# Kernel optimization log

Measured on AMD Instinct MI355X. Metric: run time of the kernel, lower is better.

The kernel has to match this reference:

```python
import jax, jax.numpy as jnp
import numpy as np

GRID = 20            # grid_size -> n1 = 400 nodes
CTX = 64             # context_size
HID = 10 * CTX       # hidden_dim per module code
BATCH = 256
K_ITERS = 100        # Dykstra iterations approximating the exact QP solve
LEAKY_SLOPE = 0.1


def _grid_incidence(g):
    """Incidence matrix of g x g grid DAG with right/down edges (SPO benchmark)."""
    n1 = g * g
    edges = []
    for i in range(g):
        for j in range(g):
            u = i * g + j
            if j + 1 < g:
                edges.append((u, u + 1))   # right
            if i + 1 < g:
                edges.append((u, u + g))   # down
    n2 = len(edges)
    A = np.zeros((n1, n2), dtype=np.float32)
    for e, (u, v) in enumerate(edges):
        A[u, e] = 1.0    # flow leaves u
        A[v, e] = -1.0   # flow enters v
    b = np.zeros(n1, dtype=np.float32)
    b[0] = 1.0           # source
    b[-1] = -1.0         # sink
    return A, b


def setup_inputs() -> dict:
    key = jax.random.key(0)
    ks = jax.random.split(key, 5)
    A_np, b_np = _grid_incidence(GRID)
    n2 = A_np.shape[1]
    d = jax.random.normal(ks[0], (BATCH, CTX), dtype=jnp.float32)
    W1 = jax.random.normal(ks[1], (CTX, HID), dtype=jnp.float32) / np.sqrt(CTX)
    b1 = jax.random.normal(ks[2], (HID,), dtype=jnp.float32) * 0.01
    W2 = jax.random.normal(ks[3], (HID, n2), dtype=jnp.float32) / np.sqrt(HID)
    b2 = jax.random.normal(ks[4], (n2,), dtype=jnp.float32) * 0.01
    return {
        "d": d, "W1": W1, "b1": b1, "W2": W2, "b2": b2,
        "A": jnp.asarray(A_np), "b_eq": jnp.asarray(b_np),
    }


def _solve_qp(w, A, b_eq):
    """Batched min_x w'x + 0.5||x||^2 s.t. Ax=b, x>=0 == proj of -w onto the
    feasible set, via Dykstra alternating projections (affine set / orthant)."""
    M = jnp.linalg.pinv(A @ A.T)  # [n1, n1]; AA' is the grid Laplacian (rank n1-1)

    def proj_affine(x):           # x: [B, n2]
        resid = x @ A.T - b_eq    # [B, n1]
        return x - (resid @ M) @ A

    y0 = -w                       # point to project
    p0 = jnp.zeros_like(w)
    q0 = jnp.zeros_like(w)

    def step(carry, _):
        y, p, q = carry
        t = y + p
        yp = proj_affine(t)
        p = t - yp
        t2 = yp + q
        y = jnp.maximum(t2, 0.0)  # projection onto x >= 0
        q = t2 - y
        return (y, p, q), None

    (y, _, _), _ = jax.lax.scan(step, (y0, p0, q0), None, length=K_ITERS)
    return y


def reference(d, W1, b1, W2, b2, A, b_eq):
    h = d @ W1 + b1
    h = jnp.where(h > 0, h, LEAKY_SLOPE * h)   # LeakyReLU(0.1)
    w = h @ W2 + b2                            # predicted edge costs [B, n2]
    return _solve_qp(w, A, b_eq)               # training-mode output: QP solution
```

## Files before the change

### kernel.cpp

```cpp
#include <hip/hip_runtime.h>
#include <math.h>

#define G 20
#define N1 400
#define N2 760
#define CTXS 64
#define HID 640
#define NB 256
#define ITERS 100
#define PI_F 3.14159265358979323846f

__device__ __forceinline__ int eR(int i, int j) { return (i < 19) ? (39 * i + 2 * j) : (741 + j); }
__device__ __forceinline__ int eD(int i, int j) { return (j < 19) ? (39 * i + 2 * j + 1) : (39 * i + 38); }

#define LOAD_ROW20(dst, base) do {                                          \
    const float4* _rp = (const float4*)(base);                              \
    float4 _r0 = _rp[0], _r1 = _rp[1], _r2 = _rp[2], _r3 = _rp[3], _r4 = _rp[4]; \
    dst[0]=_r0.x; dst[1]=_r0.y; dst[2]=_r0.z; dst[3]=_r0.w;                 \
    dst[4]=_r1.x; dst[5]=_r1.y; dst[6]=_r1.z; dst[7]=_r1.w;                 \
    dst[8]=_r2.x; dst[9]=_r2.y; dst[10]=_r2.z; dst[11]=_r2.w;               \
    dst[12]=_r3.x; dst[13]=_r3.y; dst[14]=_r3.z; dst[15]=_r3.w;             \
    dst[16]=_r4.x; dst[17]=_r4.y; dst[18]=_r4.z; dst[19]=_r4.w; } while (0)

__global__ __launch_bounds__(256, 1) void spnet_kernel(
    const float* __restrict__ dmat, const float* __restrict__ W1,
    const float* __restrict__ b1v, const float* __restrict__ W2,
    const float* __restrict__ b2v, float* __restrict__ out)
{
  const int tid = threadIdx.x;
  const int bb  = blockIdx.x;

  __shared__ __align__(16) float sdrow[CTXS];
  __shared__ __align__(16) float sh[HID];
  __shared__ __align__(16) float st0[N2];
  __shared__ __align__(16) float srowT[N1];
  __shared__ __align__(16) float sc1[N1];
  __shared__ __align__(16) float sc2T[N1];
  __shared__ __align__(16) float sd1[N1];
  __shared__ __align__(16) float szz[N1];
  __shared__ __align__(16) float tRs[G][G];
  __shared__ __align__(16) float tDs[21][G];

  for (int t = tid; t < N1; t += 256) ((float*)tRs)[t] = 0.f;
  for (int t = tid; t < 21 * G; t += 256) ((float*)tDs)[t] = 0.f;
  if (tid < CTXS) sdrow[tid] = dmat[bb * CTXS + tid];

  const bool isC = (tid < 200);
  const int c  = tid / 10;
  const int u  = tid % 10;
  const int k0 = 2 * u;

  float VA0[10], VA1[10], VC[20], S0, S1;
  {
    const float n0 = 0.22360679774997896f, nk = 0.31622776601683794f;
#pragma unroll
    for (int i = 0; i < 10; ++i) {
      VA0[i] = ((k0 == 0) ? n0 : nk) * cosf((float)(k0 * (2 * i + 1)) * (PI_F / 40.f));
      VA1[i] = nk * cosf((float)((k0 + 1) * (2 * i + 1)) * (PI_F / 40.f));
    }
#pragma unroll
    for (int k = 0; k < 20; ++k)
      VC[k] = ((k == 0) ? n0 : nk) * cosf((float)(k * (2 * u + 1)) * (PI_F / 40.f));
    float lc = 2.f - 2.f * cosf((float)c * (PI_F / 20.f));
    float l0 = 2.f - 2.f * cosf((float)k0 * (PI_F / 20.f));
    float l1 = 2.f - 2.f * cosf((float)(k0 + 1) * (PI_F / 20.f));
    S0 = (c == 0 && k0 == 0) ? 0.f : 1.f / (lc + l0);
    S1 = 1.f / (lc + l1);
  }

  __syncthreads();

  if (tid < HID / 4) {
    float4 acc = *(const float4*)(b1v + 4 * tid);
#pragma unroll 4
    for (int k = 0; k < CTXS; k += 4) {
      float4 h4 = *(const float4*)(sdrow + k);
      const float* wb = W1 + k * HID + 4 * tid;
      float4 w0 = *(const float4*)(wb);
      float4 w1 = *(const float4*)(wb + HID);
      float4 w2 = *(const float4*)(wb + 2 * HID);
      float4 w3 = *(const float4*)(wb + 3 * HID);
      acc.x = fmaf(h4.x, w0.x, acc.x); acc.y = fmaf(h4.x, w0.y, acc.y);
      acc.z = fmaf(h4.x, w0.z, acc.z); acc.w = fmaf(h4.x, w0.w, acc.w);
      acc.x = fmaf(h4.y, w1.x, acc.x); acc.y = fmaf(h4.y, w1.y, acc.y);
      acc.z = fmaf(h4.y, w1.z, acc.z); acc.w = fmaf(h4.y, w1.w, acc.w);
      acc.x = fmaf(h4.z, w2.x, acc.x); acc.y = fmaf(h4.z, w2.y, acc.y);
      acc.z = fmaf(h4.z, w2.z, acc.z); acc.w = fmaf(h4.z, w2.w, acc.w);
      acc.x = fmaf(h4.w, w3.x, acc.x); acc.y = fmaf(h4.w, w3.y, acc.y);
      acc.z = fmaf(h4.w, w3.z, acc.z); acc.w = fmaf(h4.w, w3.w, acc.w);
    }
    acc.x = acc.x > 0.f ? acc.x : 0.1f * acc.x;
    acc.y = acc.y > 0.f ? acc.y : 0.1f * acc.y;
    acc.z = acc.z > 0.f ? acc.z : 0.1f * acc.z;
    acc.w = acc.w > 0.f ? acc.w : 0.1f * acc.w;
    *(float4*)(sh + 4 * tid) = acc;
  }
  __syncthreads();

  if (tid < N2 / 4) {
    float4 acc = *(const float4*)(b2v + 4 * tid);
#pragma unroll 2
    for (int k = 0; k < HID; k += 4) {
      float4 h4 = *(const float4*)(sh + k);
      const float* wb = W2 + k * N2 + 4 * tid;
      float4 w0 = *(const float4*)(wb);
      float4 w1 = *(const float4*)(wb + N2);
      float4 w2 = *(const float4*)(wb + 2 * N2);
      float4 w3 = *(const float4*)(wb + 3 * N2);
      acc.x = fmaf(h4.x, w0.x, acc.x); acc.y = fmaf(h4.x, w0.y, acc.y);
      acc.z = fmaf(h4.x, w0.z, acc.z); acc.w = fmaf(h4.x, w0.w, acc.w);
      acc.x = fmaf(h4.y, w1.x, acc.x); acc.y = fmaf(h4.y, w1.y, acc.y);
      acc.z = fmaf(h4.y, w1.z, acc.z); acc.w = fmaf(h4.y, w1.w, acc.w);
      acc.x = fmaf(h4.z, w2.x, acc.x); acc.y = fmaf(h4.z, w2.y, acc.y);
      acc.z = fmaf(h4.z, w2.z, acc.z); acc.w = fmaf(h4.z, w2.w, acc.w);
      acc.x = fmaf(h4.w, w3.x, acc.x); acc.y = fmaf(h4.w, w3.y, acc.y);
      acc.z = fmaf(h4.w, w3.z, acc.z); acc.w = fmaf(h4.w, w3.w, acc.w);
    }
    float4 s; s.x = -acc.x; s.y = -acc.y; s.z = -acc.z; s.w = -acc.w;
    *(float4*)(st0 + 4 * tid) = s;
  }

  const int  di = tid / 5, dj4 = (tid % 5) * 4;
  const bool dAct = (tid < 100) && (di < 19);
  float dT[4], dQ[4], dY[4];
  const int  rid = tid - 128;
  const bool isR = (rid >= 0 && rid < 100);
  const int  ri = isR ? (rid / 5) : 0, rj4 = isR ? ((rid % 5) * 4) : 0;
  float rT[4], rQ[4], rY[4];
#pragma unroll
  for (int m = 0; m < 4; ++m) { dT[m]=0.f; dQ[m]=0.f; dY[m]=0.f; rT[m]=0.f; rQ[m]=0.f; rY[m]=0.f; }

  __syncthreads();

  if (dAct) {
#pragma unroll
    for (int m = 0; m < 4; ++m) dT[m] = st0[eD(di, dj4 + m)];
    *(float4*)&tDs[di + 1][dj4] = make_float4(dT[0], dT[1], dT[2], dT[3]);
  }
  if (isR) {
#pragma unroll
    for (int m = 0; m < 4; ++m) {
      int j = rj4 + m;
      rT[m] = (j < 19) ? st0[eR(ri, j)] : 0.f;
    }
    *(float4*)&tRs[ri][rj4] = make_float4(rT[0], rT[1], rT[2], rT[3]);
  }
  __syncthreads();

  for (int it = 0; it < ITERS; ++it) {
    if (isR) {
      float4 oR = *(const float4*)&tRs[ri][rj4];
      float  lf = (rj4 > 0) ? tRs[ri][rj4 - 1] : 0.f;
      float4 oD = *(const float4*)&tDs[ri + 1][rj4];
      float4 iD = *(const float4*)&tDs[ri][rj4];
      float r0 = oR.x + oD.x - lf   - iD.x;
      float r1 = oR.y + oD.y - oR.x - iD.y;
      float r2 = oR.z + oD.z - oR.y - iD.z;
      float r3 = oR.w + oD.w - oR.z - iD.w;
      if (ri == 0  && rj4 == 0)  r0 -= 1.f;
      if (ri == 19 && rj4 == 16) r3 += 1.f;
      srowT[(rj4 + 0) * G + ri] = r0;
      srowT[(rj4 + 1) * G + ri] = r1;
      srowT[(rj4 + 2) * G + ri] = r2;
      srowT[(rj4 + 3) * G + ri] = r3;
    }
    __syncthreads();

    if (isC) {
      float d_[20]; LOAD_ROW20(d_, srowT + 20 * c);
      float a0 = 0.f, a1 = 0.f;
#pragma unroll
      for (int i = 0; i < 10; ++i) {
        float e_ = d_[i] + d_[19 - i], o_ = d_[i] - d_[19 - i];
        a0 = fmaf(VA0[i], e_, a0);
        a1 = fmaf(VA1[i], o_, a1);
      }
      sc1[k0 * G + c] = a0;
      sc1[(k0 + 1) * G + c] = a1;
    }
    __syncthreads();

    if (isC) {
      float d_[20]; LOAD_ROW20(d_, sc1 + 20 * c);
      float a0 = 0.f, a1 = 0.f;
#pragma unroll
      for (int j = 0; j < 10; ++j) {
        float e_ = d_[j] + d_[19 - j], o_ = d_[j] - d_[19 - j];
        a0 = fmaf(VA0[j], e_, a0);
        a1 = fmaf(VA1[j], o_, a1);
      }
      sc2T[k0 * G + c] = a0 * S0;
      sc2T[(k0 + 1) * G + c] = a1 * S1;
    }
    __syncthreads();

    if (isC) {
      float d_[20]; LOAD_ROW20(d_, sc2T + 20 * c);
      float E = 0.f, O = 0.f;
#pragma unroll
      for (int m = 0; m < 10; ++m) {
        E = fmaf(VC[2 * m], d_[2 * m], E);
        O = fmaf(VC[2 * m + 1], d_[2 * m + 1], O);
      }
      sd1[u * G + c] = E + O;
      sd1[(19 - u) * G + c] = E - O;
    }
    __syncthreads();

    if (isC) {
      float d_[20]; LOAD_ROW20(d_, sd1 + 20 * c);
      float E = 0.f, O = 0.f;
#pragma unroll
      for (int m = 0; m < 10; ++m) {
        E = fmaf(VC[2 * m], d_[2 * m], E);
        O = fmaf(VC[2 * m + 1], d_[2 * m + 1], O);
      }
      szz[c * G + u] = E + O;
      szz[c * G + (19 - u)] = E - O;
    }
    __syncthreads();

    if (isR) {
      float4 z4 = *(const float4*)&szz[ri * G + rj4];
      float  zR = (rj4 < 16) ? szz[ri * G + rj4 + 4] : 0.f;
      float pn[4] = {z4.x - z4.y, z4.y - z4.z, z4.z - z4.w, z4.w - zR};
      if (rj4 == 16) pn[3] = 0.f;
#pragma unroll
      for (int m = 0; m < 4; ++m) {
        float t2 = rT[m] - pn[m] + rQ[m];
        float yn = fmaxf(t2, 0.f);
        rQ[m] = t2 - yn; rY[m] = yn; rT[m] = yn + pn[m];
      }
      *(float4*)&tRs[ri][rj4] = make_float4(rT[0], rT[1], rT[2], rT[3]);
    }
    if (dAct) {
      float4 z4 = *(const float4*)&szz[di * G + dj4];
      float4 zb = *(const float4*)&szz[(di + 1) * G + dj4];
      float pn[4] = {z4.x - zb.x, z4.y - zb.y, z4.z - zb.z, z4.w - zb.w};
#pragma unroll
      for (int m = 0; m < 4; ++m) {
        float t2 = dT[m] - pn[m] + dQ[m];
        float yn = fmaxf(t2, 0.f);
        dQ[m] = t2 - yn; dY[m] = yn; dT[m] = yn + pn[m];
      }
      *(float4*)&tDs[di + 1][dj4] = make_float4(dT[0], dT[1], dT[2], dT[3]);
    }
    __syncthreads();
  }

  float* mine = out + bb * N2;
  if (isR) {
#pragma unroll
    for (int m = 0; m < 4; ++m) {
      int j = rj4 + m;
      if (j < 19) mine[eR(ri, j)] = rY[m];
    }
  }
  if (dAct) {
#pragma unroll
    for (int m = 0; m < 4; ++m) mine[eD(di, dj4 + m)] = dY[m];
  }
}

extern "C" void kernel_launch(void* const* d_in, const int* in_sizes, int n_in,
                              void* d_out, int out_size, void* d_ws, size_t ws_size,
                              hipStream_t stream) {
  const float* d   = (const float*)d_in[0];
  const float* W1  = (const float*)d_in[1];
  const float* b1  = (const float*)d_in[2];
  const float* W2  = (const float*)d_in[3];
  const float* b2  = (const float*)d_in[4];
  float* out = (float*)d_out;
  spnet_kernel<<<NB, 256, 0, stream>>>(d, W1, b1, W2, b2, out);
}
```

Measured before the change: 213.8 us.

## Run Dykstra iterations in a single wavefront, replacing barriers with waitcnt and shuffles

After the MLP, the block drops to one 64-lane wavefront that owns all edge state in registers and does the DCT-based Laplacian solve with each lane covering four columns. The per-stage __syncthreads barriers become s_waitcnt lgkmcnt(0), and neighbour edge values come from cross-lane shuffles instead of shared-memory tiles. This removes about six block barriers per iteration and the tRs/tDs shared buffers. In exchange, each lane does about four times more DCT work and the loop uses only one wave per CU. It also relies on LDS ordering within a single wavefront, which is implicit and fragile.

After: 324.8 us. 51.9% more time.

```diff
diff --git a/kernel.cpp b/kernel.cpp
--- a/kernel.cpp
+++ b/kernel.cpp
@@ -13,6 +13,8 @@
 __device__ __forceinline__ int eR(int i, int j) { return (i < 19) ? (39 * i + 2 * j) : (741 + j); }
 __device__ __forceinline__ int eD(int i, int j) { return (j < 19) ? (39 * i + 2 * j + 1) : (39 * i + 38); }
 
+#define WAIT_LDS() asm volatile("s_waitcnt lgkmcnt(0)" ::: "memory")
+
 #define LOAD_ROW20(dst, base) do {                                          \
     const float4* _rp = (const float4*)(base);                              \
     float4 _r0 = _rp[0], _r1 = _rp[1], _r2 = _rp[2], _r3 = _rp[3], _r4 = _rp[4]; \
@@ -22,6 +24,11 @@
     dst[12]=_r3.x; dst[13]=_r3.y; dst[14]=_r3.z; dst[15]=_r3.w;             \
     dst[16]=_r4.x; dst[17]=_r4.y; dst[18]=_r4.z; dst[19]=_r4.w; } while (0)
 
+__device__ __forceinline__ void fma4v(float4& acc, float s, const float4& v) {
+  acc.x = fmaf(s, v.x, acc.x); acc.y = fmaf(s, v.y, acc.y);
+  acc.z = fmaf(s, v.z, acc.z); acc.w = fmaf(s, v.w, acc.w);
+}
+
 __global__ __launch_bounds__(256, 1) void spnet_kernel(
     const float* __restrict__ dmat, const float* __restrict__ W1,
     const float* __restrict__ b1v, const float* __restrict__ W2,
@@ -38,36 +45,8 @@
   __shared__ __align__(16) float sc2T[N1];
   __shared__ __align__(16) float sd1[N1];
   __shared__ __align__(16) float szz[N1];
-  __shared__ __align__(16) float tRs[G][G];
-  __shared__ __align__(16) float tDs[21][G];
-
-  for (int t = tid; t < N1; t += 256) ((float*)tRs)[t] = 0.f;
-  for (int t = tid; t < 21 * G; t += 256) ((float*)tDs)[t] = 0.f;
+
   if (tid < CTXS) sdrow[tid] = dmat[bb * CTXS + tid];
-
-  const bool isC = (tid < 200);
-  const int c  = tid / 10;
-  const int u  = tid % 10;
-  const int k0 = 2 * u;
-
-  float VA0[10], VA1[10], VC[20], S0, S1;
-  {
-    const float n0 = 0.22360679774997896f, nk = 0.31622776601683794f;
-#pragma unroll
-    for (int i = 0; i < 10; ++i) {
-      VA0[i] = ((k0 == 0) ? n0 : nk) * cosf((float)(k0 * (2 * i + 1)) * (PI_F / 40.f));
-      VA1[i] = nk * cosf((float)((k0 + 1) * (2 * i + 1)) * (PI_F / 40.f));
-    }
-#pragma unroll
-    for (int k = 0; k < 20; ++k)
-      VC[k] = ((k == 0) ? n0 : nk) * cosf((float)(k * (2 * u + 1)) * (PI_F / 40.f));
-    float lc = 2.f - 2.f * cosf((float)c * (PI_F / 20.f));
-    float l0 = 2.f - 2.f * cosf((float)k0 * (PI_F / 20.f));
-    float l1 = 2.f - 2.f * cosf((float)(k0 + 1) * (PI_F / 20.f));
-    S0 = (c == 0 && k0 == 0) ? 0.f : 1.f / (lc + l0);
-    S1 = 1.f / (lc + l1);
-  }
-
   __syncthreads();
 
   if (tid < HID / 4) {
@@ -80,14 +59,8 @@
       float4 w1 = *(const float4*)(wb + HID);
       float4 w2 = *(const float4*)(wb + 2 * HID);
       float4 w3 = *(const float4*)(wb + 3 * HID);
-      acc.x = fmaf(h4.x, w0.x, acc.x); acc.y = fmaf(h4.x, w0.y, acc.y);
-      acc.z = fmaf(h4.x, w0.z, acc.z); acc.w = fmaf(h4.x, w0.w, acc.w);
-      acc.x = fmaf(h4.y, w1.x, acc.x); acc.y = fmaf(h4.y, w1.y, acc.y);
-      acc.z = fmaf(h4.y, w1.z, acc.z); acc.w = fmaf(h4.y, w1.w, acc.w);
-      acc.x = fmaf(h4.z, w2.x, acc.x); acc.y = fmaf(h4.z, w2.y, acc.y);
-      acc.z = fmaf(h4.z, w2.z, acc.z); acc.w = fmaf(h4.z, w2.w, acc.w);
-      acc.x = fmaf(h4.w, w3.x, acc.x); acc.y = fmaf(h4.w, w3.y, acc.y);
-      acc.z = fmaf(h4.w, w3.z, acc.z); acc.w = fmaf(h4.w, w3.w, acc.w);
+      fma4v(acc, h4.x, w0); fma4v(acc, h4.y, w1);
+      fma4v(acc, h4.z, w2); fma4v(acc, h4.w, w3);
     }
     acc.x = acc.x > 0.f ? acc.x : 0.1f * acc.x;
     acc.y = acc.y > 0.f ? acc.y : 0.1f * acc.y;
@@ -107,158 +80,205 @@
       float4 w1 = *(const float4*)(wb + N2);
       float4 w2 = *(const float4*)(wb + 2 * N2);
       float4 w3 = *(const float4*)(wb + 3 * N2);
-      acc.x = fmaf(h4.x, w0.x, acc.x); acc.y = fmaf(h4.x, w0.y, acc.y);
-      acc.z = fmaf(h4.x, w0.z, acc.z); acc.w = fmaf(h4.x, w0.w, acc.w);
-      acc.x = fmaf(h4.y, w1.x, acc.x); acc.y = fmaf(h4.y, w1.y, acc.y);
-      acc.z = fmaf(h4.y, w1.z, acc.z); acc.w = fmaf(h4.y, w1.w, acc.w);
-      acc.x = fmaf(h4.z, w2.x, acc.x); acc.y = fmaf(h4.z, w2.y, acc.y);
-      acc.z = fmaf(h4.z, w2.z, acc.z); acc.w = fmaf(h4.z, w2.w, acc.w);
-      acc.x = fmaf(h4.w, w3.x, acc.x); acc.y = fmaf(h4.w, w3.y, acc.y);
-      acc.z = fmaf(h4.w, w3.z, acc.z); acc.w = fmaf(h4.w, w3.w, acc.w);
+      fma4v(acc, h4.x, w0); fma4v(acc, h4.y, w1);
+      fma4v(acc, h4.z, w2); fma4v(acc, h4.w, w3);
     }
     float4 s; s.x = -acc.x; s.y = -acc.y; s.z = -acc.z; s.w = -acc.w;
     *(float4*)(st0 + 4 * tid) = s;
   }
-
-  const int  di = tid / 5, dj4 = (tid % 5) * 4;
-  const bool dAct = (tid < 100) && (di < 19);
-  float dT[4], dQ[4], dY[4];
-  const int  rid = tid - 128;
-  const bool isR = (rid >= 0 && rid < 100);
-  const int  ri = isR ? (rid / 5) : 0, rj4 = isR ? ((rid % 5) * 4) : 0;
-  float rT[4], rQ[4], rY[4];
-#pragma unroll
-  for (int m = 0; m < 4; ++m) { dT[m]=0.f; dQ[m]=0.f; dY[m]=0.f; rT[m]=0.f; rQ[m]=0.f; rY[m]=0.f; }
-
   __syncthreads();
 
-  if (dAct) {
-#pragma unroll
-    for (int m = 0; m < 4; ++m) dT[m] = st0[eD(di, dj4 + m)];
-    *(float4*)&tDs[di + 1][dj4] = make_float4(dT[0], dT[1], dT[2], dT[3]);
-  }
-  if (isR) {
-#pragma unroll
-    for (int m = 0; m < 4; ++m) {
-      int j = rj4 + m;
-      rT[m] = (j < 19) ? st0[eR(ri, j)] : 0.f;
-    }
-    *(float4*)&tRs[ri][rj4] = make_float4(rT[0], rT[1], rT[2], rT[3]);
-  }
-  __syncthreads();
+  if (tid >= 64) return;
+  const int ln = tid;
+
+  const int  r = ln >> 1, h = ln & 1, j0 = 10 * h;
+  const bool eAct = (ln < 40);
+  const bool rOK  = (r < 19);
+  float tR[10], qR[10], tD[10], qD[10], yR[10], yD[10];
+#pragma unroll
+  for (int m = 0; m < 10; ++m) { tR[m]=0.f; qR[m]=0.f; tD[m]=0.f; qD[m]=0.f; yR[m]=0.f; yD[m]=0.f; }
+  if (eAct) {
+#pragma unroll
+    for (int m = 0; m < 10; ++m) {
+      int j = j0 + m;
+      if ((h == 0) || (m < 9)) tR[m] = st0[eR(r, j)];
+      if (rOK)                 tD[m] = st0[eD(r, j)];
+    }
+  }
+
+  const bool cAct = (ln < 50);
+  int du = ln / 5; if (du > 9) du = 9;
+  const int dg = ln % 5;
+  const int k0 = 2 * du;
+  float VA0[10], VA1[10], VC[20], S0v[4], S1v[4];
+  {
+    const float n0 = 0.22360679774997896f, nk = 0.31622776601683794f;
+#pragma unroll
+    for (int i = 0; i < 10; ++i) {
+      VA0[i] = ((k0 == 0) ? n0 : nk) * cosf((float)(k0 * (2 * i + 1)) * (PI_F / 40.f));
+      VA1[i] = nk * cosf((float)((k0 + 1) * (2 * i + 1)) * (PI_F / 40.f));
+    }
+#pragma unroll
+    for (int k = 0; k < 20; ++k)
+      VC[k] = ((k == 0) ? n0 : nk) * cosf((float)(k * (2 * du + 1)) * (PI_F / 40.f));
+    float l0 = 2.f - 2.f * cosf((float)k0 * (PI_F / 20.f));
+    float l1 = 2.f - 2.f * cosf((float)(k0 + 1) * (PI_F / 20.f));
+#pragma unroll
+    for (int cc = 0; cc < 4; ++cc) {
+      int c = 4 * dg + cc;
+      float lc = 2.f - 2.f * cosf((float)c * (PI_F / 20.f));
+      S0v[cc] = (c == 0 && k0 == 0) ? 0.f : 1.f / (lc + l0);
+      S1v[cc] = 1.f / (lc + l1);
+    }
+  }
+
+  {
+    float tDup[10];
+#pragma unroll
+    for (int m = 0; m < 10; ++m) tDup[m] = __shfl(tD[m], (ln >= 2) ? ln - 2 : ln, 64);
+    float tRl = __shfl(tR[9], (ln >= 1) ? ln - 1 : ln, 64);
+    if (eAct) {
+      float rr[10];
+#pragma unroll
+      for (int m = 0; m < 10; ++m) {
+        float inR = (m == 0) ? ((h == 0) ? 0.f : tRl) : tR[m - 1];
+        float inD = (r == 0) ? 0.f : tDup[m];
+        rr[m] = tR[m] + tD[m] - inR - inD;
+      }
+      if (r == 0  && h == 0) rr[0] -= 1.f;
+      if (r == 19 && h == 1) rr[9] += 1.f;
+#pragma unroll
+      for (int m = 0; m < 10; ++m) srowT[(j0 + m) * G + r] = rr[m];
+    }
+  }
+  WAIT_LDS();
 
   for (int it = 0; it < ITERS; ++it) {
-    if (isR) {
-      float4 oR = *(const float4*)&tRs[ri][rj4];
-      float  lf = (rj4 > 0) ? tRs[ri][rj4 - 1] : 0.f;
-      float4 oD = *(const float4*)&tDs[ri + 1][rj4];
-      float4 iD = *(const float4*)&tDs[ri][rj4];
-      float r0 = oR.x + oD.x - lf   - iD.x;
-      float r1 = oR.y + oD.y - oR.x - iD.y;
-      float r2 = oR.z + oD.z - oR.y - iD.z;
-      float r3 = oR.w + oD.w - oR.z - iD.w;
-      if (ri == 0  && rj4 == 0)  r0 -= 1.f;
-      if (ri == 19 && rj4 == 16) r3 += 1.f;
-      srowT[(rj4 + 0) * G + ri] = r0;
-      srowT[(rj4 + 1) * G + ri] = r1;
-      srowT[(rj4 + 2) * G + ri] = r2;
-      srowT[(rj4 + 3) * G + ri] = r3;
-    }
-    __syncthreads();
-
-    if (isC) {
-      float d_[20]; LOAD_ROW20(d_, srowT + 20 * c);
-      float a0 = 0.f, a1 = 0.f;
-#pragma unroll
-      for (int i = 0; i < 10; ++i) {
-        float e_ = d_[i] + d_[19 - i], o_ = d_[i] - d_[19 - i];
-        a0 = fmaf(VA0[i], e_, a0);
-        a1 = fmaf(VA1[i], o_, a1);
-      }
-      sc1[k0 * G + c] = a0;
-      sc1[(k0 + 1) * G + c] = a1;
-    }
-    __syncthreads();
-
-    if (isC) {
-      float d_[20]; LOAD_ROW20(d_, sc1 + 20 * c);
-      float a0 = 0.f, a1 = 0.f;
-#pragma unroll
-      for (int j = 0; j < 10; ++j) {
-        float e_ = d_[j] + d_[19 - j], o_ = d_[j] - d_[19 - j];
-        a0 = fmaf(VA0[j], e_, a0);
-        a1 = fmaf(VA1[j], o_, a1);
-      }
-      sc2T[k0 * G + c] = a0 * S0;
-      sc2T[(k0 + 1) * G + c] = a1 * S1;
-    }
-    __syncthreads();
-
-    if (isC) {
-      float d_[20]; LOAD_ROW20(d_, sc2T + 20 * c);
-      float E = 0.f, O = 0.f;
+    if (cAct) {
+#pragma unroll
+      for (int cc = 0; cc < 4; ++cc) {
+        const int c = 4 * dg + cc;
+        float d_[20]; LOAD_ROW20(d_, srowT + 20 * c);
+        float a0 = 0.f, a1 = 0.f;
+#pragma unroll
+        for (int i = 0; i < 10; ++i) {
+          float e_ = d_[i] + d_[19 - i], o_ = d_[i] - d_[19 - i];
+          a0 = fmaf(VA0[i], e_, a0);
+          a1 = fmaf(VA1[i], o_, a1);
+        }
+        sc1[k0 * G + c] = a0;
+        sc1[(k0 + 1) * G + c] = a1;
+      }
+    }
+    WAIT_LDS();
+
+    if (cAct) {
+#pragma unroll
+      for (int cc = 0; cc < 4; ++cc) {
+        const int c = 4 * dg + cc;
+        float d_[20]; LOAD_ROW20(d_, sc1 + 20 * c);
+        float a0 = 0.f, a1 = 0.f;
+#pragma unroll
+        for (int j = 0; j < 10; ++j) {
+          float e_ = d_[j] + d_[19 - j], o_ = d_[j] - d_[19 - j];
+          a0 = fmaf(VA0[j], e_, a0);
+          a1 = fmaf(VA1[j], o_, a1);
+        }
+        sc2T[k0 * G + c] = a0 * S0v[cc];
+        sc2T[(k0 + 1) * G + c] = a1 * S1v[cc];
+      }
+    }
+    WAIT_LDS();
+
+    if (cAct) {
+#pragma unroll
+      for (int cc = 0; cc < 4; ++cc) {
+        const int c = 4 * dg + cc;
+        float d_[20]; LOAD_ROW20(d_, sc2T + 20 * c);
+        float E = 0.f, O = 0.f;
+#pragma unroll
+        for (int m = 0; m < 10; ++m) {
+          E = fmaf(VC[2 * m], d_[2 * m], E);
+          O = fmaf(VC[2 * m + 1], d_[2 * m + 1], O);
+        }
+        sd1[du * G + c] = E + O;
+        sd1[(19 - du) * G + c] = E - O;
+      }
+    }
+    WAIT_LDS();
+
+    if (cAct) {
+#pragma unroll
+      for (int cc = 0; cc < 4; ++cc) {
+        const int c = 4 * dg + cc;
+        float d_[20]; LOAD_ROW20(d_, sd1 + 20 * c);
+        float E = 0.f, O = 0.f;
+#pragma unroll
+        for (int m = 0; m < 10; ++m) {
+          E = fmaf(VC[2 * m], d_[2 * m], E);
+          O = fmaf(VC[2 * m + 1], d_[2 * m + 1], O);
+        }
+        szz[c * G + du] = E + O;
+        szz[c * G + (19 - du)] = E - O;
+      }
+    }
+    WAIT_LDS();
+
+    if (eAct) {
+      const int zb = r * G + j0;
+      float zi[11], zd[10];
+#pragma unroll
+      for (int m = 0; m < 10; ++m) zi[m] = szz[zb + m];
+      { int a10 = zb + 10; if (a10 > 399) a10 = 399; zi[10] = szz[a10]; }
+      const int zb2 = (rOK ? (r + 1) : r) * G + j0;
+#pragma unroll
+      for (int m = 0; m < 10; ++m) zd[m] = szz[zb2 + m];
 #pragma unroll
       for (int m = 0; m < 10; ++m) {
-        E = fmaf(VC[2 * m], d_[2 * m], E);
-        O = fmaf(VC[2 * m + 1], d_[2 * m + 1], O);
-      }
-      sd1[u * G + c] = E + O;
-      sd1[(19 - u) * G + c] = E - O;
-    }
-    __syncthreads();
-
-    if (isC) {
-      float d_[20]; LOAD_ROW20(d_, sd1 + 20 * c);
-      float E = 0.f, O = 0.f;
+        bool vR = (h == 0) || (m < 9);
+        float pn = vR ? (zi[m] - zi[m + 1]) : 0.f;
+        float t2 = tR[m] - pn + qR[m];
+        float yn = fmaxf(t2, 0.f);
+        qR[m] = t2 - yn; yR[m] = yn; tR[m] = yn + pn;
+      }
 #pragma unroll
       for (int m = 0; m < 10; ++m) {
-        E = fmaf(VC[2 * m], d_[2 * m], E);
-        O = fmaf(VC[2 * m + 1], d_[2 * m + 1], O);
-      }
-      szz[c * G + u] = E + O;
-      szz[c * G + (19 - u)] = E - O;
-    }
-    __syncthreads();
-
-    if (isR) {
-      float4 z4 = *(const float4*)&szz[ri * G + rj4];
-      float  zR = (rj4 < 16) ? szz[ri * G + rj4 + 4] : 0.f;
-      float pn[4] = {z4.x - z4.y, z4.y - z4.z, z4.z - z4.w, z4.w - zR};
-      if (rj4 == 16) pn[3] = 0.f;
-#pragma unroll
-      for (int m = 0; m < 4; ++m) {
-        float t2 = rT[m] - pn[m] + rQ[m];
+        float pn = rOK ? (zi[m] - zd[m]) : 0.f;
+        float t2 = tD[m] - pn + qD[m];
         float yn = fmaxf(t2, 0.f);
-        rQ[m] = t2 - yn; rY[m] = yn; rT[m] = yn + pn[m];
-      }
-      *(float4*)&tRs[ri][rj4] = make_float4(rT[0], rT[1], rT[2], rT[3]);
-    }
-    if (dAct) {
-      float4 z4 = *(const float4*)&szz[di * G + dj4];
-      float4 zb = *(const float4*)&szz[(di + 1) * G + dj4];
-      float pn[4] = {z4.x - zb.x, z4.y - zb.y, z4.z - zb.z, z4.w - zb.w};
-#pragma unroll
-      for (int m = 0; m < 4; ++m) {
-        float t2 = dT[m] - pn[m] + dQ[m];
-        float yn = fmaxf(t2, 0.f);
-        dQ[m] = t2 - yn; dY[m] = yn; dT[m] = yn + pn[m];
-      }
-      *(float4*)&tDs[di + 1][dj4] = make_float4(dT[0], dT[1], dT[2], dT[3]);
-    }
-    __syncthreads();
-  }
-
-  float* mine = out + bb * N2;
-  if (isR) {
-#pragma unroll
-    for (int m = 0; m < 4; ++m) {
-      int j = rj4 + m;
-      if (j < 19) mine[eR(ri, j)] = rY[m];
-    }
-  }
-  if (dAct) {
-#pragma unroll
-    for (int m = 0; m < 4; ++m) mine[eD(di, dj4 + m)] = dY[m];
+        qD[m] = t2 - yn; yD[m] = yn; tD[m] = yn + pn;
+      }
+    }
+    if (it < ITERS - 1) {
+      float tDup[10];
+#pragma unroll
+      for (int m = 0; m < 10; ++m) tDup[m] = __shfl(tD[m], (ln >= 2) ? ln - 2 : ln, 64);
+      float tRl = __shfl(tR[9], (ln >= 1) ? ln - 1 : ln, 64);
+      if (eAct) {
+        float rr[10];
+#pragma unroll
+        for (int m = 0; m < 10; ++m) {
+          float inR = (m == 0) ? ((h == 0) ? 0.f : tRl) : tR[m - 1];
+          float inD = (r == 0) ? 0.f : tDup[m];
+          rr[m] = tR[m] + tD[m] - inR - inD;
+        }
+        if (r == 0  && h == 0) rr[0] -= 1.f;
+        if (r == 19 && h == 1) rr[9] += 1.f;
+#pragma unroll
+        for (int m = 0; m < 10; ++m) srowT[(j0 + m) * G + r] = rr[m];
+      }
+      WAIT_LDS();
+    }
+  }
+
+  if (eAct) {
+    float* mine = out + bb * N2;
+#pragma unroll
+    for (int m = 0; m < 10; ++m) {
+      int j = j0 + m;
+      if ((h == 0) || (m < 9)) mine[eR(r, j)] = yR[m];
+      if (rOK)                 mine[eD(r, j)] = yD[m];
+    }
   }
 }
 
```
